# Performance work log

Hardware: AMD Instinct MI355X
Metric: run time of the kernel (lower is better)

The kernel has to match this reference:

```python
import jax, jax.numpy as jnp
import numpy as np

K = 3          # kernel_size
EPS = 1e-5     # BatchNorm eps


def setup_inputs() -> dict:
    key = jax.random.key(0)
    k1, k2, k3 = jax.random.split(key, 3)
    n, C, H, W = 8, 64, 128, 128
    x = jax.random.normal(k1, (n, C, H, W), dtype=jnp.float32)
    conv_w = jax.random.normal(k2, (C * K * K, C), dtype=jnp.float32) * np.sqrt(2.0 / (C * K * K))
    bn_gamma = jnp.ones((C * K * K,), dtype=jnp.float32)
    bn_beta = jnp.zeros((C * K * K,), dtype=jnp.float32)
    bn_mean = jnp.zeros((C * K * K,), dtype=jnp.float32)
    bn_var = jax.random.uniform(k3, (C * K * K,), dtype=jnp.float32)
    return {"x": x, "conv_w": conv_w, "bn_gamma": bn_gamma, "bn_beta": bn_beta,
            "bn_mean": bn_mean, "bn_var": bn_var}


def reference(x, conv_w, bn_gamma, bn_beta, bn_mean, bn_var):
    n, C, H, W = x.shape
    # ---- per-image dynamic filter: GAP -> 1x1 conv -> BN (eval) -> softmax over k^2 ----
    f = x.mean(axis=(2, 3))                       # (n, C)
    f = f @ conv_w.T                              # (n, C*9)  (1x1 conv on 1x1 map, no bias)
    f = (f - bn_mean) * (bn_gamma / jnp.sqrt(bn_var + EPS)) + bn_beta
    f = jax.nn.softmax(f.reshape(n, C, K * K), axis=-1)   # softmax over kernel positions
    # ---- reflect-pad + unfold (im2col), row-major kernel offsets matching F.unfold ----
    xp = jnp.pad(x, ((0, 0), (0, 0), (1, 1), (1, 1)), mode="reflect")
    patches = jnp.stack([xp[:, :, i:i + H, j:j + W]
                         for i in range(K) for j in range(K)], axis=2)  # (n, C, 9, H, W)
    # ---- softmax-weighted dynamic sum over the 9 taps ----
    out = jnp.einsum("nckhw,nck->nchw", patches, f)
    return out, x - out
```

## Files before the change

### kernel.cpp

```cpp
#include <hip/hip_runtime.h>

#define WW 128
#define HWSZ 16384
#define CC 64
#define NPLANE 512
#define NCHW 8388608
#define BN_EPS 1e-5f
#define TAG_MAGIC 0x5A5A5A5Au

typedef float v4f __attribute__((ext_vector_type(4)));

__global__ __launch_bounds__(256, 2) void dc_fused_kernel(
        const float* __restrict__ x,
        const float* __restrict__ conv_w,
        const float* __restrict__ gamma,
        const float* __restrict__ beta,
        const float* __restrict__ bn_mean,
        const float* __restrict__ bn_var,
        float* __restrict__ out,
        unsigned int* __restrict__ ws) {
    unsigned int* bits = ws;
    unsigned int* tag  = ws + NPLANE;
    const int plane = blockIdx.x;
    const int tid   = threadIdx.x;
    const int g     = tid >> 5;
    const int q     = tid & 31;
    const int w0    = q * 4;
    const int n = plane >> 6;
    const int c = plane & 63;
    const float* xpl = x + (size_t)plane * HWSZ;

    __shared__ float haloT[8][WW];
    __shared__ float haloB[8][WW];
    __shared__ float lv9[9];
    __shared__ float wsum[4];
    __shared__ float sums[CC];

    v4f xr[16];
    float s = 0.f;
#pragma unroll
    for (int i = 0; i < 16; ++i) {
        xr[i] = *(const v4f*)(xpl + (size_t)(g * 16 + i) * WW + w0);
        s += xr[i].x + xr[i].y + xr[i].z + xr[i].w;
    }
    *(v4f*)(&haloT[g][w0]) = xr[0];
    *(v4f*)(&haloB[g][w0]) = xr[15];

    for (int off = 32; off > 0; off >>= 1)
        s += __shfl_down(s, off, 64);
    if ((tid & 63) == 0) wsum[tid >> 6] = s;
    __syncthreads();

    if (tid == 0) {
        unsigned int b = __float_as_uint(wsum[0] + wsum[1] + wsum[2] + wsum[3]);
        __hip_atomic_store(&bits[plane], b, __ATOMIC_RELAXED, __HIP_MEMORY_SCOPE_AGENT);
        __hip_atomic_store(&tag[plane], b ^ TAG_MAGIC, __ATOMIC_RELEASE, __HIP_MEMORY_SCOPE_AGENT);
    }

    if (tid < CC) {
        const int p = (n << 6) | tid;
        unsigned int b = 0, t = 0;
        int budget = 1 << 16;
        for (;;) {
            t = __hip_atomic_load(&tag[p],  __ATOMIC_ACQUIRE, __HIP_MEMORY_SCOPE_AGENT);
            b = __hip_atomic_load(&bits[p], __ATOMIC_RELAXED, __HIP_MEMORY_SCOPE_AGENT);
            if (t == (b ^ TAG_MAGIC) || --budget == 0) break;
        }
        float sv;
        if (t == (b ^ TAG_MAGIC)) {
            sv = __uint_as_float(b);
        } else {
            const v4f* xq = (const v4f*)(x + (size_t)p * HWSZ);
            float fs = 0.f;
            for (int i = 0; i < HWSZ / 4; ++i) {
                v4f v = xq[i];
                fs += v.x + v.y + v.z + v.w;
            }
            sv = fs;
        }
        sums[tid] = sv;
    }
    __syncthreads();

    if (tid < 144) {
        const int j    = tid >> 4;
        const int part = tid & 15;
        const int jj = c * 9 + j;
        v4f ps = *(const v4f*)(&sums[part * 4]);
        v4f wv = *(const v4f*)(conv_w + (size_t)jj * CC + part * 4);
        float d = ps.x * wv.x + ps.y * wv.y + ps.z * wv.z + ps.w * wv.w;
        d += __shfl_down(d, 8, 16);
        d += __shfl_down(d, 4, 16);
        d += __shfl_down(d, 2, 16);
        d += __shfl_down(d, 1, 16);
        if (part == 0) {
            d *= (1.0f / 16384.0f);
            const float gm = gamma[jj] * rsqrtf(bn_var[jj] + BN_EPS);
            lv9[j] = (d - bn_mean[jj]) * gm + beta[jj];
        }
    }
    __syncthreads();

    float w9[9];
    {
        float m = lv9[0];
#pragma unroll
        for (int t = 1; t < 9; ++t) m = fmaxf(m, lv9[t]);
        float den = 0.f;
        float e[9];
#pragma unroll
        for (int t = 0; t < 9; ++t) { e[t] = __expf(lv9[t] - m); den += e[t]; }
        const float inv = 1.0f / den;
#pragma unroll
        for (int t = 0; t < 9; ++t) w9[t] = e[t] * inv;
    }

#define EDGES(c4, e0, e1)                                                   \
    {                                                                       \
        float lft = __shfl_up(c4.w, 1, 32);                                 \
        float rgt = __shfl_down(c4.x, 1, 32);                               \
        e0 = (w0 == 0)   ? c4.y : lft;           \
        e1 = (w0 == 124) ? c4.z : rgt;          \
    }
#define HALO(buf, gg, c4, e0, e1)                                           \
    {                                                                       \
        const float* hr = buf[gg];                                          \
        c4 = *(const v4f*)(hr + w0);                                        \
        e0 = (w0 == 0)   ? hr[1]   : hr[w0 - 1];                            \
        e1 = (w0 == 124) ? hr[126] : hr[w0 + 4];                            \
    }

    v4f cP, cC, cN;
    float eP0, eP1, eC0, eC1, eN0, eN1;

    if (g == 0) { cP = xr[1]; EDGES(cP, eP0, eP1); }
    else        { HALO(haloB, g - 1, cP, eP0, eP1); }
    cC = xr[0]; EDGES(cC, eC0, eC1);
    cN = xr[1]; EDGES(cN, eN0, eN1);

    const int r0 = g * 16;
#pragma unroll
    for (int i = 0; i < 16; ++i) {
        const float VP[6] = {eP0, cP.x, cP.y, cP.z, cP.w, eP1};
        const float VC[6] = {eC0, cC.x, cC.y, cC.z, cC.w, eC1};
        const float VN[6] = {eN0, cN.x, cN.y, cN.z, cN.w, eN1};

        float o[4];
#pragma unroll
        for (int p = 0; p < 4; ++p) {
            float acc = 0.f;
#pragma unroll
            for (int t = 0; t < 3; ++t) {
                acc = fmaf(w9[t],     VP[p + t], acc);
                acc = fmaf(w9[3 + t], VC[p + t], acc);
                acc = fmaf(w9[6 + t], VN[p + t], acc);
            }
            o[p] = acc;
        }

        const size_t base = (size_t)plane * HWSZ + (size_t)(r0 + i) * WW + w0;
        v4f ov = {o[0], o[1], o[2], o[3]};
        v4f dv = {cC.x - o[0], cC.y - o[1], cC.z - o[2], cC.w - o[3]};
        __builtin_nontemporal_store(ov, (v4f*)(out + base));
        __builtin_nontemporal_store(dv, (v4f*)(out + NCHW + base));

        if (i < 15) {
            cP = cC; eP0 = eC0; eP1 = eC1;
            cC = cN; eC0 = eN0; eC1 = eN1;
            if (i == 14) {
                if (g == 7) { cN = xr[14]; EDGES(cN, eN0, eN1); }
                else        { HALO(haloT, g + 1, cN, eN0, eN1); }
            } else {
                cN = xr[i + 2]; EDGES(cN, eN0, eN1);
            }
        }
    }
#undef EDGES
#undef HALO
}

extern "C" void kernel_launch(void* const* d_in, const int* in_sizes, int n_in,
                              void* d_out, int out_size, void* d_ws, size_t ws_size,
                              hipStream_t stream) {
    const float* x       = (const float*)d_in[0];
    const float* conv_w  = (const float*)d_in[1];
    const float* gamma   = (const float*)d_in[2];
    const float* beta    = (const float*)d_in[3];
    const float* bn_mean = (const float*)d_in[4];
    const float* bn_var  = (const float*)d_in[5];
    float* out = (float*)d_out;
    unsigned int* ws = (unsigned int*)d_ws;

    dc_fused_kernel<<<NPLANE, 256, 0, stream>>>(x, conv_w, gamma, beta,
                                                bn_mean, bn_var, out, ws);
}
```

Baseline: 120.9 us.

## Split each plane into four row bands and sync per-image via atomic counters

Each plane is now processed by four blocks, each owning 32 rows, which gives 2048 blocks and allows higher occupancy (launch bounds raised to 8). Per-band partial sums go to a workspace, and a per-image atomic counter (zeroed by a memset before launch) replaces the per-plane tag handshake. Each block spins until all 256 bands of its image have arrived, then reads the partials. This relies on all blocks of an image being co-resident, and falls back to recomputing the plane sums if a spin budget expires. The change adds a memset launch and an extra halo-row load per band.

```diff
diff --git a/kernel.cpp b/kernel.cpp
--- a/kernel.cpp
+++ b/kernel.cpp
@@ -6,11 +6,10 @@
 #define NPLANE 512
 #define NCHW 8388608
 #define BN_EPS 1e-5f
-#define TAG_MAGIC 0x5A5A5A5Au
 
 typedef float v4f __attribute__((ext_vector_type(4)));
 
-__global__ __launch_bounds__(256, 2) void dc_fused_kernel(
+__global__ __launch_bounds__(256, 8) void dc_fused_kernel(
         const float* __restrict__ x,
         const float* __restrict__ conv_w,
         const float* __restrict__ gamma,
@@ -18,10 +17,11 @@
         const float* __restrict__ bn_mean,
         const float* __restrict__ bn_var,
         float* __restrict__ out,
-        unsigned int* __restrict__ ws) {
-    unsigned int* bits = ws;
-    unsigned int* tag  = ws + NPLANE;
-    const int plane = blockIdx.x;
+        unsigned int* __restrict__ cnt,
+        float* __restrict__ partial) {
+    const int b     = blockIdx.x;
+    const int plane = b >> 2;
+    const int band  = b & 3;
     const int tid   = threadIdx.x;
     const int g     = tid >> 5;
     const int q     = tid & 31;
@@ -29,22 +29,35 @@
     const int n = plane >> 6;
     const int c = plane & 63;
     const float* xpl = x + (size_t)plane * HWSZ;
+    const int r0 = band * 32 + g * 4;
 
     __shared__ float haloT[8][WW];
     __shared__ float haloB[8][WW];
     __shared__ float lv9[9];
     __shared__ float wsum[4];
     __shared__ float sums[CC];
-
-    v4f xr[16];
+    __shared__ int okf;
+
+    v4f xr[4];
     float s = 0.f;
 #pragma unroll
-    for (int i = 0; i < 16; ++i) {
-        xr[i] = *(const v4f*)(xpl + (size_t)(g * 16 + i) * WW + w0);
+    for (int i = 0; i < 4; ++i) {
+        xr[i] = *(const v4f*)(xpl + (size_t)(r0 + i) * WW + w0);
         s += xr[i].x + xr[i].y + xr[i].z + xr[i].w;
     }
     *(v4f*)(&haloT[g][w0]) = xr[0];
-    *(v4f*)(&haloB[g][w0]) = xr[15];
+    *(v4f*)(&haloB[g][w0]) = xr[3];
+
+    v4f hEdge; float hE0, hE1;
+    {
+        const int R  = (g == 0) ? (r0 - 1) : ((g == 7) ? (r0 + 4) : r0);
+        const int RR = (R < 0) ? 1 : ((R > 127) ? 126 : R);
+        hEdge = *(const v4f*)(xpl + (size_t)RR * WW + w0);
+        float lft = __shfl_up(hEdge.w, 1, 32);
+        float rgt = __shfl_down(hEdge.x, 1, 32);
+        hE0 = (w0 == 0)   ? hEdge.y : lft;
+        hE1 = (w0 == 124) ? hEdge.z : rgt;
+    }
 
     for (int off = 32; off > 0; off >>= 1)
         s += __shfl_down(s, off, 64);
@@ -52,25 +65,28 @@
     __syncthreads();
 
     if (tid == 0) {
-        unsigned int b = __float_as_uint(wsum[0] + wsum[1] + wsum[2] + wsum[3]);
-        __hip_atomic_store(&bits[plane], b, __ATOMIC_RELAXED, __HIP_MEMORY_SCOPE_AGENT);
-        __hip_atomic_store(&tag[plane], b ^ TAG_MAGIC, __ATOMIC_RELEASE, __HIP_MEMORY_SCOPE_AGENT);
-    }
+        partial[b] = wsum[0] + wsum[1] + wsum[2] + wsum[3];
+        __threadfence();
+        atomicAdd(&cnt[n << 5], 1u);
+        int ok = 0;
+        int budget = 1 << 15;
+        do {
+            if (__hip_atomic_load(&cnt[n << 5], __ATOMIC_ACQUIRE,
+                                  __HIP_MEMORY_SCOPE_AGENT) >= 256u) { ok = 1; break; }
+            __builtin_amdgcn_s_sleep(2);
+        } while (--budget);
+        okf = ok;
+    }
+    __syncthreads();
 
     if (tid < CC) {
-        const int p = (n << 6) | tid;
-        unsigned int b = 0, t = 0;
-        int budget = 1 << 16;
-        for (;;) {
-            t = __hip_atomic_load(&tag[p],  __ATOMIC_ACQUIRE, __HIP_MEMORY_SCOPE_AGENT);
-            b = __hip_atomic_load(&bits[p], __ATOMIC_RELAXED, __HIP_MEMORY_SCOPE_AGENT);
-            if (t == (b ^ TAG_MAGIC) || --budget == 0) break;
-        }
         float sv;
-        if (t == (b ^ TAG_MAGIC)) {
-            sv = __uint_as_float(b);
+        if (okf) {
+            const int p4 = ((n << 6) | tid) << 2;
+            v4f pv = *(const v4f*)(partial + p4);
+            sv = pv.x + pv.y + pv.z + pv.w;
         } else {
-            const v4f* xq = (const v4f*)(x + (size_t)p * HWSZ);
+            const v4f* xq = (const v4f*)(x + (size_t)((n << 6) | tid) * HWSZ);
             float fs = 0.f;
             for (int i = 0; i < HWSZ / 4; ++i) {
                 v4f v = xq[i];
@@ -133,14 +149,13 @@
     v4f cP, cC, cN;
     float eP0, eP1, eC0, eC1, eN0, eN1;
 
-    if (g == 0) { cP = xr[1]; EDGES(cP, eP0, eP1); }
+    if (g == 0) { cP = hEdge; eP0 = hE0; eP1 = hE1; }
     else        { HALO(haloB, g - 1, cP, eP0, eP1); }
     cC = xr[0]; EDGES(cC, eC0, eC1);
     cN = xr[1]; EDGES(cN, eN0, eN1);
 
-    const int r0 = g * 16;
-#pragma unroll
-    for (int i = 0; i < 16; ++i) {
+#pragma unroll
+    for (int i = 0; i < 4; ++i) {
         const float VP[6] = {eP0, cP.x, cP.y, cP.z, cP.w, eP1};
         const float VC[6] = {eC0, cC.x, cC.y, cC.z, cC.w, eC1};
         const float VN[6] = {eN0, cN.x, cN.y, cN.z, cN.w, eN1};
@@ -164,11 +179,11 @@
         __builtin_nontemporal_store(ov, (v4f*)(out + base));
         __builtin_nontemporal_store(dv, (v4f*)(out + NCHW + base));
 
-        if (i < 15) {
+        if (i < 3) {
             cP = cC; eP0 = eC0; eP1 = eC1;
             cC = cN; eC0 = eN0; eC1 = eN1;
-            if (i == 14) {
-                if (g == 7) { cN = xr[14]; EDGES(cN, eN0, eN1); }
+            if (i == 2) {
+                if (g == 7) { cN = hEdge; eN0 = hE0; eN1 = hE1; }
                 else        { HALO(haloT, g + 1, cN, eN0, eN1); }
             } else {
                 cN = xr[i + 2]; EDGES(cN, eN0, eN1);
@@ -189,8 +204,11 @@
     const float* bn_mean = (const float*)d_in[4];
     const float* bn_var  = (const float*)d_in[5];
     float* out = (float*)d_out;
-    unsigned int* ws = (unsigned int*)d_ws;
-
-    dc_fused_kernel<<<NPLANE, 256, 0, stream>>>(x, conv_w, gamma, beta,
-                                                bn_mean, bn_var, out, ws);
+    unsigned int* cnt = (unsigned int*)d_ws;
+    float* partial = (float*)d_ws + 256;
+
+    hipMemsetAsync(d_ws, 0, 1024, stream);
+    dc_fused_kernel<<<NPLANE * 4, 256, 0, stream>>>(x, conv_w, gamma, beta,
+                                                    bn_mean, bn_var, out,
+                                                    cnt, partial);
 }
```

Measured after the change: 251.5 us. 108% more time.
